# Performance work log

Hardware: AMD Instinct MI355X
Metric: run time of the kernel (lower is better)

Reference implementation:

```python
import jax, jax.numpy as jnp
import numpy as np

B, S, D = 2, 2048, 2048
H, HKV, HD = 32, 8, 64
G = H // HKV  # num_key_value_groups


def setup_inputs() -> dict:
    key = jax.random.key(0)
    ks = jax.random.split(key, 9)
    sc = 0.02
    return {
        "x": jax.random.normal(ks[0], (B, S, D), jnp.float32),
        "wq": jax.random.normal(ks[1], (H * HD, D), jnp.float32) * sc,
        "bq": jax.random.normal(ks[2], (H * HD,), jnp.float32) * sc,
        "wk": jax.random.normal(ks[3], (HKV * HD, D), jnp.float32) * sc,
        "bk": jax.random.normal(ks[4], (HKV * HD,), jnp.float32) * sc,
        "wv": jax.random.normal(ks[5], (HKV * HD, D), jnp.float32) * sc,
        "bv": jax.random.normal(ks[6], (HKV * HD,), jnp.float32) * sc,
        "wo": jax.random.normal(ks[7], (D, H * HD), jnp.float32) * sc,
        "bo": jax.random.normal(ks[8], (D,), jnp.float32) * sc,
    }


def reference(x, wq, bq, wk, bk, wv, bv, wo, bo):
    b, s, _ = x.shape
    # fused-QKV-style projections (nn.Linear: x @ W.T + b)
    q = (jnp.einsum("bsd,ed->bse", x, wq) + bq).reshape(b, s, H, HD)
    k = (jnp.einsum("bsd,ed->bse", x, wk) + bk).reshape(b, s, HKV, HD)
    v = (jnp.einsum("bsd,ed->bse", x, wv) + bv).reshape(b, s, HKV, HD)
    # (B, Hkv, G, S, hd): grouped query heads share a KV head — same math as
    # repeat_kv (expand+flatten) without materializing the expanded KV tensor
    q = q.transpose(0, 2, 1, 3).reshape(b, HKV, G, s, HD)
    k = k.transpose(0, 2, 1, 3)  # (B, Hkv, S, hd)
    v = v.transpose(0, 2, 1, 3)
    scale = 1.0 / jnp.sqrt(jnp.asarray(HD, x.dtype))
    scores = jnp.einsum("bkgqd,bktd->bkgqt", q, k) * scale  # (B,Hkv,G,S,S)
    causal = jnp.tril(jnp.ones((s, s), bool))
    scores = jnp.where(causal, scores, jnp.asarray(-jnp.inf, scores.dtype))
    probs = jax.nn.softmax(scores, axis=-1)
    o = jnp.einsum("bkgqt,bktd->bkgqd", probs, v)  # (B,Hkv,G,S,hd)
    o = o.reshape(b, H, s, HD).transpose(0, 2, 1, 3).reshape(b, s, H * HD)
    return jnp.einsum("bse,de->bsd", o, wo) + bo
```

## Files before the change

### kernel.cpp

```cpp
#include <hip/hip_runtime.h>
#include <hip/hip_bf16.h>
#include <cmath>

#define B_   2
#define S_   2048
#define D_   2048
#define H_   32
#define HKV_ 8
#define HD_  64

using bf16 = __hip_bfloat16;
typedef __bf16    bf16x8 __attribute__((ext_vector_type(8)));
typedef float     floatx4 __attribute__((ext_vector_type(4)));
typedef _Float16  half4 __attribute__((ext_vector_type(4)));

#if __has_builtin(__builtin_amdgcn_exp2f)
#define EXP2(x) __builtin_amdgcn_exp2f(x)
#else
#define EXP2(x) exp2f(x)
#endif

#define QSCALE 0.18033688011112042f

__device__ inline void async16(const void* g, void* l) {
  __builtin_amdgcn_global_load_lds(
      (const __attribute__((address_space(1))) void*)g,
      (__attribute__((address_space(3))) void*)l, 16, 0, 0);
}

#define MFMA32B(a, b, c) __builtin_amdgcn_mfma_f32_16x16x32_bf16((a), (b), (c), 0, 0, 0)
#define MFMA16H(a, b, c) __builtin_amdgcn_mfma_f32_16x16x16f16((a), (b), (c), 0, 0, 0)

__global__ void f2b_all(const float* __restrict__ x,  const float* __restrict__ wq,
                        const float* __restrict__ wk, const float* __restrict__ wv,
                        const float* __restrict__ wo,
                        bf16* __restrict__ xb,  bf16* __restrict__ wqb,
                        bf16* __restrict__ wkb, bf16* __restrict__ wvb,
                        bf16* __restrict__ wob) {
  const int i = blockIdx.x * blockDim.x + threadIdx.x;
  const float* src; bf16* dst; int off; float scale = 1.0f;
  if (i < 1048576)      { src = x;  dst = xb;  off = 0; }
  else if (i < 1572864) { src = wq; dst = wqb; off = 1048576; scale = QSCALE; }
  else if (i < 1703936) { src = wk; dst = wkb; off = 1572864; }
  else if (i < 1835008) { src = wv; dst = wvb; off = 1703936; }
  else                  { src = wo; dst = wob; off = 1835008; }
  const int j = i - off;
  float4 a  = ((const float4*)src)[2 * j];
  float4 b2 = ((const float4*)src)[2 * j + 1];
  alignas(16) bf16 t[8];
  t[0] = __float2bfloat16(a.x * scale);  t[1] = __float2bfloat16(a.y * scale);
  t[2] = __float2bfloat16(a.z * scale);  t[3] = __float2bfloat16(a.w * scale);
  t[4] = __float2bfloat16(b2.x * scale); t[5] = __float2bfloat16(b2.y * scale);
  t[6] = __float2bfloat16(b2.z * scale); t[7] = __float2bfloat16(b2.w * scale);
  ((uint4*)dst)[j] = *(const uint4*)t;
}

__device__ inline void gemm_body(const bf16* __restrict__ Ag, const bf16* __restrict__ Bg,
                                 const float* __restrict__ bias,
                                 float* __restrict__ C, int Ncol, int K, int bm, int colb,
                                 bf16* As, bf16* Bs) {
  const int tid  = threadIdx.x;
  const int wid  = tid >> 6, lane = tid & 63;
  const int lm   = lane & 15, quad = lane >> 4;
  const int wm   = (wid >> 1) * 64, wn = (wid & 1) * 64;

  floatx4 acc[4][4] = {};

  const int l0 = tid * 8;
  const int r0 = l0 >> 5, c0 = l0 & 31;
  const int r1 = r0 + 64;

  for (int k0 = 0; k0 < K; k0 += 32) {
    async16(Ag + (size_t)r0 * K + k0 + c0, &As[l0]);
    async16(Ag + (size_t)r1 * K + k0 + c0, &As[l0 + 2048]);
    async16(Bg + (size_t)r0 * K + k0 + c0, &Bs[l0]);
    async16(Bg + (size_t)r1 * K + k0 + c0, &Bs[l0 + 2048]);
    asm volatile("s_waitcnt vmcnt(0)" ::: "memory");
    __syncthreads();

    bf16x8 aF[4], bF[4];
#pragma unroll
    for (int mi = 0; mi < 4; ++mi)
      aF[mi] = *(const bf16x8*)&As[(wm + mi * 16 + lm) * 32 + quad * 8];
#pragma unroll
    for (int ni = 0; ni < 4; ++ni)
      bF[ni] = *(const bf16x8*)&Bs[(wn + ni * 16 + lm) * 32 + quad * 8];
#pragma unroll
    for (int mi = 0; mi < 4; ++mi)
#pragma unroll
      for (int ni = 0; ni < 4; ++ni)
        acc[mi][ni] = MFMA32B(bF[ni], aF[mi], acc[mi][ni]);
    __syncthreads();
  }

#pragma unroll
  for (int mi = 0; mi < 4; ++mi) {
    const int row = bm * 128 + wm + mi * 16 + lm;
#pragma unroll
    for (int ni = 0; ni < 4; ++ni) {
      const int col0 = colb + wn + ni * 16 + quad * 4;
      float4 bv4 = *(const float4*)&bias[col0];
      float4 o4;
      o4.x = acc[mi][ni][0] + bv4.x; o4.y = acc[mi][ni][1] + bv4.y;
      o4.z = acc[mi][ni][2] + bv4.z; o4.w = acc[mi][ni][3] + bv4.w;
      *(float4*)&C[(size_t)row * Ncol + col0] = o4;
    }
  }
}

__global__ __launch_bounds__(256, 2)
void gemm_o(const bf16* __restrict__ A, const bf16* __restrict__ Bm,
            const float* __restrict__ bias, float* __restrict__ C,
            int Ncol, int K) {
  __shared__ bf16 As[128 * 32];
  __shared__ bf16 Bs[128 * 32];
  const int bn = blockIdx.x, bm = blockIdx.y;
  gemm_body(A + (size_t)bm * 128 * K, Bm + (size_t)bn * 128 * K, bias,
            C, Ncol, K, bm, bn * 128, As, Bs);
}

__global__ __launch_bounds__(512, 2)
void gemm_qkv8(const bf16* __restrict__ xb, const bf16* __restrict__ Wcat,
               const float* __restrict__ bq, const float* __restrict__ bk,
               const float* __restrict__ bv,
               bf16* __restrict__ Qo, bf16* __restrict__ Ko,
               _Float16* __restrict__ VG) {
  constexpr int NT = D_ / 64;
  __shared__ bf16 L[65536];

  const int id = blockIdx.x;
  const int bn = id & 7;
  const int bm = id >> 3;

  const int tid = threadIdx.x;
  const int wid = tid >> 6, lane = tid & 63;
  const int lm = lane & 15, quad = lane >> 4;
  const int wm = wid >> 2, wn = wid & 3;

  const int cOff = (quad * 8) ^ (((lm >> 3) & 1) << 4);
  const bf16* LA0 = L + (wm * 64 + lm) * 32 + cOff;
  const bf16* LB0 = L + 8192 + (wn * 96 + lm) * 32 + cOff;

  const int r0 = tid >> 2;
  const int csrc = ((tid & 3) * 8) ^ (((tid >> 5) & 1) << 4);
  const bf16* Asrc = xb   + (size_t)(bm * 128 + r0) * D_ + csrc;
  const bf16* Bs0  = Wcat + (size_t)(bn * 384 + r0) * D_ + csrc;
  const bf16* Bs1  = Bs0 + (size_t)128 * D_;
  const bf16* Bs2  = Bs0 + (size_t)256 * D_;
  bf16* Ld = L + tid * 8;

  floatx4 acc[4][6] = {};

#define BARX() { asm volatile("" ::: "memory"); __builtin_amdgcn_s_barrier(); \
                 asm volatile("" ::: "memory"); }
#define LGKM0() asm volatile("s_waitcnt lgkmcnt(0)" ::: "memory")
#define STG_A(tt, hh, DB)  async16(Asrc + (tt) * 64 + (hh) * 32, (DB) + (hh) * 4096)
#define STG_B0(tt, hh, DB) async16(Bs0  + (tt) * 64 + (hh) * 32, (DB) + 8192 + (hh) * 12288)
#define STG_B1(tt, hh, DB) async16(Bs1  + (tt) * 64 + (hh) * 32, (DB) + 8192 + (hh) * 12288 + 4096)
#define STG_B2(tt, hh, DB) async16(Bs2  + (tt) * 64 + (hh) * 32, (DB) + 8192 + (hh) * 12288 + 8192)

  STG_A(0, 0, Ld); STG_B0(0, 0, Ld); STG_B1(0, 0, Ld); STG_B2(0, 0, Ld);
  STG_A(0, 1, Ld); STG_B0(0, 1, Ld); STG_B1(0, 1, Ld); STG_B2(0, 1, Ld);
  STG_A(1, 0, Ld + 32768); STG_B0(1, 0, Ld + 32768);
  STG_B1(1, 0, Ld + 32768); STG_B2(1, 0, Ld + 32768);
  asm volatile("s_waitcnt vmcnt(8)" ::: "memory");
  BARX();

  auto tile = [&](int t, const int BUF) __attribute__((always_inline)) {
    const bf16* LA = LA0 + BUF;
    const bf16* LB = LB0 + BUF;
    bf16* SD  = Ld + BUF;
    bf16* SDo = Ld + (BUF ^ 32768);
    const bool s1 = (t + 1) < NT, s2 = (t + 2) < NT;
    bf16x8 aF[4], bF[3];

#pragma unroll
    for (int i = 0; i < 4; ++i) aF[i] = *(const bf16x8*)(LA + i * 512);
#pragma unroll
    for (int i = 0; i < 3; ++i) bF[i] = *(const bf16x8*)(LB + i * 512);
    if (s1) { STG_A(t + 1, 1, SDo); STG_B0(t + 1, 1, SDo); }
    BARX(); LGKM0();
    __builtin_amdgcn_s_setprio(1);
#pragma unroll
    for (int mi = 0; mi < 4; ++mi)
#pragma unroll
      for (int ni = 0; ni < 3; ++ni)
        acc[mi][ni] = MFMA32B(bF[ni], aF[mi], acc[mi][ni]);
    __builtin_amdgcn_s_setprio(0);
    BARX();

#pragma unroll
    for (int i = 0; i < 3; ++i) bF[i] = *(const bf16x8*)(LB + (i + 3) * 512);
    if (s1) { STG_B1(t + 1, 1, SDo); STG_B2(t + 1, 1, SDo); }
    BARX(); LGKM0();
    __builtin_amdgcn_s_setprio(1);
#pragma unroll
    for (int mi = 0; mi < 4; ++mi)
#pragma unroll
      for (int ni = 0; ni < 3; ++ni)
        acc[mi][ni + 3] = MFMA32B(bF[ni], aF[mi], acc[mi][ni + 3]);
    __builtin_amdgcn_s_setprio(0);
    if (s1) { asm volatile("s_waitcnt vmcnt(8)" ::: "memory"); }
    else    { asm volatile("s_waitcnt vmcnt(0)" ::: "memory"); }
    BARX();

#pragma unroll
    for (int i = 0; i < 4; ++i) aF[i] = *(const bf16x8*)(LA + 4096 + i * 512);
#pragma unroll
    for (int i = 0; i < 3; ++i) bF[i] = *(const bf16x8*)(LB + 12288 + i * 512);
    if (s2) { STG_A(t + 2, 0, SD); STG_B0(t + 2, 0, SD); }
    BARX(); LGKM0();
    __builtin_amdgcn_s_setprio(1);
#pragma unroll
    for (int mi = 0; mi < 4; ++mi)
#pragma unroll
      for (int ni = 0; ni < 3; ++ni)
        acc[mi][ni] = MFMA32B(bF[ni], aF[mi], acc[mi][ni]);
    __builtin_amdgcn_s_setprio(0);
    BARX();

#pragma unroll
    for (int i = 0; i < 3; ++i) bF[i] = *(const bf16x8*)(LB + 12288 + (i + 3) * 512);
    if (s2) { STG_B1(t + 2, 0, SD); STG_B2(t + 2, 0, SD); }
    BARX(); LGKM0();
    __builtin_amdgcn_s_setprio(1);
#pragma unroll
    for (int mi = 0; mi < 4; ++mi)
#pragma unroll
      for (int ni = 0; ni < 3; ++ni)
        acc[mi][ni + 3] = MFMA32B(bF[ni], aF[mi], acc[mi][ni + 3]);
    __builtin_amdgcn_s_setprio(0);
    if (s2)      { asm volatile("s_waitcnt vmcnt(8)" ::: "memory"); }
    else if (s1) { asm volatile("s_waitcnt vmcnt(4)" ::: "memory"); }
    else         { asm volatile("s_waitcnt vmcnt(0)" ::: "memory"); }
    BARX();
  };

  for (int t = 0; t < NT; t += 2) { tile(t, 0); tile(t + 1, 32768); }

#undef BARX
#undef LGKM0
#undef STG_A
#undef STG_B0
#undef STG_B1
#undef STG_B2

#pragma unroll
  for (int mi = 0; mi < 4; ++mi) {
    const int row = bm * 128 + wm * 64 + mi * 16 + lm;
#pragma unroll
    for (int ni = 0; ni < 6; ++ni) {
      const int colf = bn * 384 + wn * 96 + ni * 16;
      const int col0 = colf + quad * 4;
      if (colf < 2048) {
        float4 bv4 = *(const float4*)&bq[col0];
        alignas(8) bf16 t4[4];
#pragma unroll
        for (int r = 0; r < 4; ++r)
          t4[r] = __float2bfloat16(acc[mi][ni][r] + ((const float*)&bv4)[r] * QSCALE);
        *(uint2*)&Qo[(size_t)row * (H_ * HD_) + col0] = *(const uint2*)t4;
      } else if (colf < 2560) {
        const int ck = col0 - 2048;
        float4 bv4 = *(const float4*)&bk[ck];
        alignas(8) bf16 t4[4];
#pragma unroll
        for (int r = 0; r < 4; ++r)
          t4[r] = __float2bfloat16(acc[mi][ni][r] + ((const float*)&bv4)[r]);
        *(uint2*)&Ko[(size_t)row * (HKV_ * HD_) + ck] = *(const uint2*)t4;
      } else {
        const int cv = col0 - 2560;
        const int kvh = cv >> 6, hd = cv & 63;
        const int nh = hd >> 4;
        const int bb = row >> 11, s2 = row & 2047;
        const int tl = s2 >> 6, kvin = s2 & 63;
        const int kc = kvin >> 4, qd = (kvin >> 2) & 3, j = kvin & 3;
        const size_t base = ((size_t)((bb * 8 + kvh) * 32 + tl) << 12) +
                            (((kc * 4 + nh) * 4 + qd) << 6) + j;
        float4 bv4 = *(const float4*)&bv[cv];
#pragma unroll
        for (int r = 0; r < 4; ++r)
          VG[base + (size_t)(quad * 4 + r) * 4] =
              (_Float16)(acc[mi][ni][r] + ((const float*)&bv4)[r]);
      }
    }
  }
}

__global__ __launch_bounds__(256, 4)
void attn_kernel(const bf16* __restrict__ Q, const bf16* __restrict__ K,
                 const _Float16* __restrict__ VG, bf16* __restrict__ O) {
  const int tid = threadIdx.x;
  const int wid = tid >> 6, lane = tid & 63;
  const int lm = lane & 15, quad = lane >> 4;

  const int n   = blockIdx.y * 64 + blockIdx.x;
  const int x3  = n & 7, b1 = (n >> 3) & 1;
  const int pair = n >> 4;
  const int grp  = x3 * 2 + b1;
  const int b    = grp >> 3, kvh = grp & 7;
  const int head = kvh * 4 + wid;

  const int hi = 127 - pair, lo = pair;
  const int nt_hi = (hi >> 2) + 1;
  const int nt_lo = (lo >> 2) + 1;

  __shared__ bf16     Ks[2 * 64 * 64];
  __shared__ _Float16 Vs[2 * 64 * 64];

  const int tb[2] = {hi * 16, lo * 16};

  bf16x8 qf[2][2];
#pragma unroll
  for (int tt = 0; tt < 2; ++tt) {
    const size_t qg = ((size_t)(b * S_ + tb[tt] + lm)) * (H_ * HD_) + head * HD_;
#pragma unroll
    for (int kf = 0; kf < 2; ++kf)
      qf[tt][kf] = *(const bf16x8*)&Q[qg + kf * 32 + quad * 8];
  }

  half4 onesh;
#pragma unroll
  for (int j = 0; j < 4; ++j) onesh[j] = (_Float16)1.0f;

  floatx4 o_acc[2][4] = {};
  floatx4 lacc[2] = {};

  const int tr = tid >> 2;
  const int tc = (tid & 3) * 8;

  auto stage = [&](int t, int buf) {
#pragma unroll
    for (int c = 0; c < 2; ++c) {
      async16(&K[(size_t)(b * S_ + t * 64 + tr) * (HKV_ * HD_) + kvh * HD_ + c * 32 + tc],
              &Ks[buf * 4096 + c * 2048 + tid * 8]);
      async16(&VG[((size_t)(grp * 32 + t) << 12) + c * 2048 + tid * 8],
              &Vs[buf * 4096 + c * 2048 + tid * 8]);
    }
  };

  stage(0, 0);

  for (int t = 0; t < nt_hi; ++t) {
    const int cur = t & 1;
    asm volatile("s_waitcnt vmcnt(0)" ::: "memory");
    __syncthreads();
    if (t + 1 < nt_hi) stage(t + 1, cur ^ 1);

    const bf16*     Kb = &Ks[cur * 4096];
    const _Float16* Vb = &Vs[cur * 4096];
    const int t0 = t * 64;
    const int nact = (t < nt_lo) ? 2 : 1;

    int kcmax[2], kcross[2];
#pragma unroll
    for (int tt = 0; tt < 2; ++tt) {
      const int rel = tb[tt] + 15 - t0;
      kcmax[tt]  = (tt < nact) ? ((rel >> 4) >= 3 ? 4 : (rel >> 4) + 1) : 0;
      kcross[tt] = rel >> 4;
    }

    half4 pb[2][4];
#pragma unroll
    for (int kc = 0; kc < 4; ++kc) {
      if (kc >= kcmax[0]) break;
      bf16x8 kb0 = *(const bf16x8*)&Kb[(kc * 16 + lm) * 32 + quad * 8];
      bf16x8 kb1 = *(const bf16x8*)&Kb[2048 + (kc * 16 + lm) * 32 + quad * 8];
#pragma unroll
      for (int tt = 0; tt < 2; ++tt) {
        if (kc >= kcmax[tt]) continue;
        floatx4 sT = {};
        sT = MFMA32B(kb0, qf[tt][0], sT);
        sT = MFMA32B(kb1, qf[tt][1], sT);
        half4 pk;
        if (kc == kcross[tt]) {
          const int qrel = tb[tt] + lm - t0;
#pragma unroll
          for (int r = 0; r < 4; ++r) {
            float p = (kc * 16 + quad * 4 + r > qrel) ? 0.f : EXP2(sT[r]);
            pk[r] = (_Float16)p;
          }
        } else {
#pragma unroll
          for (int r = 0; r < 4; ++r) pk[r] = (_Float16)EXP2(sT[r]);
        }
        pb[tt][kc] = pk;
      }
    }

#pragma unroll
    for (int tt = 0; tt < 2; ++tt) {
      if (kcmax[tt] == 0) continue;
      half4 ps = pb[tt][0];
      if (kcmax[tt] > 1) ps += pb[tt][1];
      if (kcmax[tt] > 2) ps += pb[tt][2];
      if (kcmax[tt] > 3) ps += pb[tt][3];
      lacc[tt] = MFMA16H(onesh, ps, lacc[tt]);
    }

#pragma unroll
    for (int kc = 0; kc < 4; ++kc) {
      if (kc >= kcmax[0]) break;
#pragma unroll
      for (int nh = 0; nh < 4; ++nh) {
        half4 va = *(const half4*)&Vb[((kc * 4 + nh) * 4 + quad) * 64 + lm * 4];
#pragma unroll
        for (int tt = 0; tt < 2; ++tt)
          if (kc < kcmax[tt]) o_acc[tt][nh] = MFMA16H(va, pb[tt][kc], o_acc[tt][nh]);
      }
    }
  }

#pragma unroll
  for (int tt = 0; tt < 2; ++tt) {
    const float rl = 1.f / lacc[tt][0];
    const size_t rowg = (size_t)(b * S_ + tb[tt] + lm);
#pragma unroll
    for (int nh = 0; nh < 4; ++nh) {
      alignas(8) bf16 tmp[4];
#pragma unroll
      for (int r = 0; r < 4; ++r)
        tmp[r] = __float2bfloat16(o_acc[tt][nh][r] * rl);
      *(uint2*)&O[rowg * (H_ * HD_) + head * HD_ + nh * 16 + quad * 4] = *(uint2*)tmp;
    }
  }
}

extern "C" void kernel_launch(void* const* d_in, const int* in_sizes, int n_in,
                              void* d_out, int out_size, void* d_ws, size_t ws_size,
                              hipStream_t stream) {
  (void)in_sizes; (void)n_in; (void)out_size; (void)ws_size;
  const float* x  = (const float*)d_in[0];
  const float* wq = (const float*)d_in[1];
  const float* bq = (const float*)d_in[2];
  const float* wk = (const float*)d_in[3];
  const float* bk = (const float*)d_in[4];
  const float* wv = (const float*)d_in[5];
  const float* bv = (const float*)d_in[6];
  const float* wo = (const float*)d_in[7];
  const float* bo = (const float*)d_in[8];
  float* out = (float*)d_out;

  const int M = B_ * S_;
  const int E = H_ * HD_;
  const int EKV = HKV_ * HD_;

  char* ws = (char*)d_ws;
  size_t off = 0;
  auto alloc = [&](size_t bytes) {
    char* p = ws + off;
    off += (bytes + 255) & ~(size_t)255;
    return p;
  };
  bf16* xb   = (bf16*)alloc((size_t)M * D_ * 2);
  bf16* Wcat = (bf16*)alloc((size_t)(E + 2 * EKV) * D_ * 2);
  bf16* wob  = (bf16*)alloc((size_t)D_ * E * 2);
  bf16* Qb   = (bf16*)alloc((size_t)M * E * 2);
  bf16* Kb   = (bf16*)alloc((size_t)M * EKV * 2);
  _Float16* VG = (_Float16*)alloc((size_t)M * EKV * 2);
  bf16* Ob   = (bf16*)alloc((size_t)M * E * 2);

  bf16* wqb = Wcat;
  bf16* wkb = Wcat + (size_t)E * D_;
  bf16* wvb = Wcat + (size_t)(E + EKV) * D_;

  f2b_all<<<9216, 256, 0, stream>>>(x, wq, wk, wv, wo, xb, wqb, wkb, wvb, wob);

  gemm_qkv8<<<dim3(256), dim3(512), 0, stream>>>(xb, Wcat, bq, bk, bv,
                                                 Qb, Kb, VG);

  attn_kernel<<<dim3(64, 16), 256, 0, stream>>>(Qb, Kb, VG, Ob);

  gemm_o<<<dim3(D_ / 128, M / 128), 256, 0, stream>>>(Ob, wob, bo, out, D_, D_);
}
```

Before: 285.0 us.

## Interleave attention QK/PV per key chunk with wider V LDS reads and setprio

Restructures the attention inner loop so each 16-key chunk computes scores, exponentiates and immediately feeds its PV MFMAs, instead of running three separate passes over all chunks. The V tile layout written by the projection kernel is changed so two head-dim slices sit adjacent, which lets one 16-byte LDS load replace two 8-byte loads. The loop also uses packed round-toward-zero fp16 conversion, masks with -inf before exp, wraps the MFMA bursts in s_setprio, and raises the launch-bounds occupancy target from 4 to 5. Together these aim to cut register pressure and LDS instructions and to overlap MFMA with the exp work, at the risk of register spills under the tighter occupancy bound.

```diff
diff --git a/kernel.cpp b/kernel.cpp
--- a/kernel.cpp
+++ b/kernel.cpp
@@ -13,6 +13,8 @@
 typedef __bf16    bf16x8 __attribute__((ext_vector_type(8)));
 typedef float     floatx4 __attribute__((ext_vector_type(4)));
 typedef _Float16  half4 __attribute__((ext_vector_type(4)));
+typedef _Float16  half8 __attribute__((ext_vector_type(8)));
+typedef _Float16  half2v __attribute__((ext_vector_type(2)));
 
 #if __has_builtin(__builtin_amdgcn_exp2f)
 #define EXP2(x) __builtin_amdgcn_exp2f(x)
@@ -26,6 +28,10 @@
   __builtin_amdgcn_global_load_lds(
       (const __attribute__((address_space(1))) void*)g,
       (__attribute__((address_space(3))) void*)l, 16, 0, 0);
+}
+
+__device__ inline half2v pkrtz(float a, float b) {
+  return __builtin_bit_cast(half2v, __builtin_amdgcn_cvt_pkrtz(a, b));
 }
 
 #define MFMA32B(a, b, c) __builtin_amdgcn_mfma_f32_16x16x32_bf16((a), (b), (c), 0, 0, 0)
@@ -275,18 +281,19 @@
         const int tl = s2 >> 6, kvin = s2 & 63;
         const int kc = kvin >> 4, qd = (kvin >> 2) & 3, j = kvin & 3;
         const size_t base = ((size_t)((bb * 8 + kvh) * 32 + tl) << 12) +
-                            (((kc * 4 + nh) * 4 + qd) << 6) + j;
+                            (size_t)(((kc * 2 + (nh >> 1)) * 4 + qd) * 128 +
+                                     (nh & 1) * 4 + j);
         float4 bv4 = *(const float4*)&bv[cv];
 #pragma unroll
         for (int r = 0; r < 4; ++r)
-          VG[base + (size_t)(quad * 4 + r) * 4] =
+          VG[base + (size_t)(quad * 4 + r) * 8] =
               (_Float16)(acc[mi][ni][r] + ((const float*)&bv4)[r]);
       }
     }
   }
 }
 
-__global__ __launch_bounds__(256, 4)
+__global__ __launch_bounds__(256, 5)
 void attn_kernel(const bf16* __restrict__ Q, const bf16* __restrict__ K,
                  const _Float16* __restrict__ VG, bf16* __restrict__ O) {
   const int tid = threadIdx.x;
@@ -325,10 +332,9 @@
   floatx4 o_acc[2][4] = {};
   floatx4 lacc[2] = {};
 
-  const int tr = tid >> 2;
-  const int tc = (tid & 3) * 8;
-
   auto stage = [&](int t, int buf) {
+    const int tr = tid >> 2;
+    const int tc = (tid & 3) * 8;
 #pragma unroll
     for (int c = 0; c < 2; ++c) {
       async16(&K[(size_t)(b * S_ + t * 64 + tr) * (HKV_ * HD_) + kvh * HD_ + c * 32 + tc],
@@ -359,55 +365,65 @@
       kcross[tt] = rel >> 4;
     }
 
-    half4 pb[2][4];
+    half4 ps[2] = {};
+
 #pragma unroll
     for (int kc = 0; kc < 4; ++kc) {
       if (kc >= kcmax[0]) break;
       bf16x8 kb0 = *(const bf16x8*)&Kb[(kc * 16 + lm) * 32 + quad * 8];
       bf16x8 kb1 = *(const bf16x8*)&Kb[2048 + (kc * 16 + lm) * 32 + quad * 8];
+
+      floatx4 sT[2];
+      __builtin_amdgcn_s_setprio(1);
 #pragma unroll
       for (int tt = 0; tt < 2; ++tt) {
         if (kc >= kcmax[tt]) continue;
-        floatx4 sT = {};
-        sT = MFMA32B(kb0, qf[tt][0], sT);
-        sT = MFMA32B(kb1, qf[tt][1], sT);
-        half4 pk;
+        floatx4 s0 = {};
+        s0 = MFMA32B(kb0, qf[tt][0], s0);
+        sT[tt] = MFMA32B(kb1, qf[tt][1], s0);
+      }
+      __builtin_amdgcn_s_setprio(0);
+
+      half8 v0 = *(const half8*)&Vb[(kc * 8 + quad) * 128 + lm * 8];
+      half8 v1 = *(const half8*)&Vb[(kc * 8 + 4 + quad) * 128 + lm * 8];
+      half4 v0l = __builtin_shufflevector(v0, v0, 0, 1, 2, 3);
+      half4 v0h = __builtin_shufflevector(v0, v0, 4, 5, 6, 7);
+      half4 v1l = __builtin_shufflevector(v1, v1, 0, 1, 2, 3);
+      half4 v1h = __builtin_shufflevector(v1, v1, 4, 5, 6, 7);
+
+      half4 pbk[2];
+#pragma unroll
+      for (int tt = 0; tt < 2; ++tt) {
+        if (kc >= kcmax[tt]) continue;
+        floatx4 s = sT[tt];
         if (kc == kcross[tt]) {
           const int qrel = tb[tt] + lm - t0;
 #pragma unroll
-          for (int r = 0; r < 4; ++r) {
-            float p = (kc * 16 + quad * 4 + r > qrel) ? 0.f : EXP2(sT[r]);
-            pk[r] = (_Float16)p;
-          }
-        } else {
-#pragma unroll
-          for (int r = 0; r < 4; ++r) pk[r] = (_Float16)EXP2(sT[r]);
+          for (int r = 0; r < 4; ++r)
+            if (kc * 16 + quad * 4 + r > qrel) s[r] = -__builtin_inff();
         }
-        pb[tt][kc] = pk;
+        half2v c0 = pkrtz(EXP2(s[0]), EXP2(s[1]));
+        half2v c1 = pkrtz(EXP2(s[2]), EXP2(s[3]));
+        half4 pk = __builtin_shufflevector(c0, c1, 0, 1, 2, 3);
+        pbk[tt] = pk;
+        ps[tt] += pk;
       }
-    }
-
-#pragma unroll
-    for (int tt = 0; tt < 2; ++tt) {
-      if (kcmax[tt] == 0) continue;
-      half4 ps = pb[tt][0];
-      if (kcmax[tt] > 1) ps += pb[tt][1];
-      if (kcmax[tt] > 2) ps += pb[tt][2];
-      if (kcmax[tt] > 3) ps += pb[tt][3];
-      lacc[tt] = MFMA16H(onesh, ps, lacc[tt]);
-    }
-
-#pragma unroll
-    for (int kc = 0; kc < 4; ++kc) {
-      if (kc >= kcmax[0]) break;
-#pragma unroll
-      for (int nh = 0; nh < 4; ++nh) {
-        half4 va = *(const half4*)&Vb[((kc * 4 + nh) * 4 + quad) * 64 + lm * 4];
-#pragma unroll
-        for (int tt = 0; tt < 2; ++tt)
-          if (kc < kcmax[tt]) o_acc[tt][nh] = MFMA16H(va, pb[tt][kc], o_acc[tt][nh]);
+
+      __builtin_amdgcn_s_setprio(1);
+#pragma unroll
+      for (int tt = 0; tt < 2; ++tt) {
+        if (kc >= kcmax[tt]) continue;
+        o_acc[tt][0] = MFMA16H(v0l, pbk[tt], o_acc[tt][0]);
+        o_acc[tt][1] = MFMA16H(v0h, pbk[tt], o_acc[tt][1]);
+        o_acc[tt][2] = MFMA16H(v1l, pbk[tt], o_acc[tt][2]);
+        o_acc[tt][3] = MFMA16H(v1h, pbk[tt], o_acc[tt][3]);
       }
-    }
+      __builtin_amdgcn_s_setprio(0);
+    }
+
+#pragma unroll
+    for (int tt = 0; tt < 2; ++tt)
+      if (kcmax[tt]) lacc[tt] = MFMA16H(onesh, ps[tt], lacc[tt]);
   }
 
 #pragma unroll
```

New measurement: 291.9 us. +2.4%, slower.
